# Performance work log

Hardware: AMD Instinct MI355X
Metric: run time of the kernel (lower is better)

The kernel has to match this reference:

```python
import jax, jax.numpy as jnp
import numpy as np

R = 32          # voxel resolution
GROUPS = 8
EPS = 1e-5


def silu(x):
    return x * jax.nn.sigmoid(x)


def group_norm(x, gamma, beta):
    # x: (B, C, *spatial); normalize over (C/G, *spatial) per group
    B, C = x.shape[0], x.shape[1]
    sp = x.shape[2:]
    xg = x.reshape(B, GROUPS, C // GROUPS, -1)
    mean = xg.mean(axis=(2, 3), keepdims=True)
    var = xg.var(axis=(2, 3), keepdims=True)
    xn = ((xg - mean) * jax.lax.rsqrt(var + EPS)).reshape(B, C, *sp)
    pshape = (1, C) + (1,) * len(sp)
    return xn * gamma.reshape(pshape) + beta.reshape(pshape)


def voxelize(x, coords):
    # x: (B, C, N), coords: (B, N, 3) in [0, 1] -> scatter-mean onto (B, C, R, R, R)
    c = coords * (R - 1)
    idx = jnp.clip(jnp.floor(c).astype(jnp.int32), 0, R - 1)
    flat = (idx[..., 0] * R + idx[..., 1]) * R + idx[..., 2]  # (B, N)

    def one(feat_cn, fi):
        sums = jax.ops.segment_sum(feat_cn.T, fi, num_segments=R ** 3)        # (R^3, C)
        cnt = jax.ops.segment_sum(jnp.ones_like(fi, dtype=feat_cn.dtype), fi,
                                  num_segments=R ** 3)                        # (R^3,)
        mean = sums / jnp.clip(cnt, 1.0)[:, None]
        return mean.T.reshape(feat_cn.shape[0], R, R, R)

    return jax.vmap(one)(x, flat)


def devoxelize(vox, coords):
    # vox: (B, C, R, R, R), coords: (B, N, 3) -> trilinear gather (B, C, N)
    B, C = vox.shape[0], vox.shape[1]
    c = coords * (R - 1)
    f = c - jnp.floor(c)                                  # fractional part (B, N, 3)
    x0 = jnp.clip(jnp.floor(c).astype(jnp.int32), 0, R - 1)
    x1 = jnp.clip(x0 + 1, 0, R - 1)
    vflat = vox.reshape(B, C, R ** 3)
    out = jnp.zeros((B, C, coords.shape[1]), dtype=vox.dtype)
    for dx in (0, 1):
        for dy in (0, 1):
            for dz in (0, 1):
                ix = x1[..., 0] if dx else x0[..., 0]
                iy = x1[..., 1] if dy else x0[..., 1]
                iz = x1[..., 2] if dz else x0[..., 2]
                w = ((f[..., 0] if dx else 1.0 - f[..., 0])
                     * (f[..., 1] if dy else 1.0 - f[..., 1])
                     * (f[..., 2] if dz else 1.0 - f[..., 2]))  # (B, N)
                fi = (ix * R + iy) * R + iz                      # (B, N)
                g = jnp.take_along_axis(vflat, fi[:, None, :], axis=2)  # (B, C, N)
                out = out + g * w[:, None, :]
    return out


def conv3d(x, w):
    # x: (B, C, D, H, W), w: (O, I, 3, 3, 3), padding 1
    return jax.lax.conv_general_dilated(
        x, w, window_strides=(1, 1, 1), padding='SAME',
        dimension_numbers=('NCDHW', 'OIDHW', 'NCDHW'))


def setup_inputs() -> dict:
    key = jax.random.key(0)
    ks = jax.random.split(key, 16)
    B, Cin, Cout, N, T = 4, 32, 64, 32768, 256
    s = 0.02
    return {
        'feats_bcn': jax.random.normal(ks[0], (B, Cin, N), jnp.float32),
        'coords_bnc3': jax.random.uniform(ks[1], (B, N, 3), jnp.float32),
        't_emb_bt': jax.random.normal(ks[2], (B, T), jnp.float32),
        'w_in': jax.random.normal(ks[3], (Cout, Cin), jnp.float32) * s,
        'gn1_g': jnp.ones((Cout,), jnp.float32), 'gn1_b': jnp.zeros((Cout,), jnp.float32),
        'w_time': jax.random.normal(ks[4], (Cout, T), jnp.float32) * s,
        'b_time': jnp.zeros((Cout,), jnp.float32),
        'w_vox1': jax.random.normal(ks[5], (Cout, Cout, 3, 3, 3), jnp.float32) * s,
        'gn2_g': jnp.ones((Cout,), jnp.float32), 'gn2_b': jnp.zeros((Cout,), jnp.float32),
        'w_vox2': jax.random.normal(ks[6], (Cout, Cout, 3, 3, 3), jnp.float32) * s,
        'gn3_g': jnp.ones((Cout,), jnp.float32), 'gn3_b': jnp.zeros((Cout,), jnp.float32),
        'w_fuse': jax.random.normal(ks[7], (Cout, Cout), jnp.float32) * s,
        'gn4_g': jnp.ones((Cout,), jnp.float32), 'gn4_b': jnp.zeros((Cout,), jnp.float32),
        'w_skip': jax.random.normal(ks[8], (Cout, Cin), jnp.float32) * s,
    }


def reference(feats_bcn, coords_bnc3, t_emb_bt, w_in, gn1_g, gn1_b, w_time, b_time,
              w_vox1, gn2_g, gn2_b, w_vox2, gn3_g, gn3_b, w_fuse, gn4_g, gn4_b, w_skip):
    # point_in: 1x1 conv1d + GN + SiLU
    x_in = silu(group_norm(jnp.einsum('oc,bcn->bon', w_in, feats_bcn), gn1_g, gn1_b))
    # time bias
    bias = (t_emb_bt @ w_time.T + b_time)[:, :, None]          # (B, C, 1)
    x_in = x_in + bias
    # scatter-mean voxelization + bias
    vox = voxelize(x_in, coords_bnc3) + bias[..., None, None]  # (B, C, R, R, R)
    # voxel conv stack
    vox = silu(group_norm(conv3d(vox, w_vox1), gn2_g, gn2_b))
    vox = silu(group_norm(conv3d(vox, w_vox2), gn3_g, gn3_b))
    # trilinear devoxelize back to points
    devox = devoxelize(vox, coords_bnc3)                        # (B, C, N)
    out = silu(group_norm(jnp.einsum('oc,bcn->bon', w_fuse, devox), gn4_g, gn4_b))
    x_skip = jnp.einsum('oc,bcn->bon', w_skip, feats_bcn)
    return out + x_skip
```

## Files before the change

### kernel.cpp

```cpp
#include <hip/hip_runtime.h>
#include <hip/hip_bf16.h>
#include <hip/hip_fp16.h>

typedef __hip_bfloat16 bf16;
typedef unsigned short u16;
typedef unsigned int u32;
typedef __attribute__((ext_vector_type(8))) short bf16x8;
typedef __attribute__((ext_vector_type(4))) float f32x4;

#define DI __device__ __forceinline__

DI float bfu2f(u32 u) { u32 v = u << 16; float f; __builtin_memcpy(&f, &v, 4); return f; }
DI u16 f2bfu(float f) { bf16 h = __float2bfloat16(f); u16 u; __builtin_memcpy(&u, &h, 2); return u; }
DI float hu2f(u32 u) { __half h; u16 s = (u16)u; __builtin_memcpy(&h, &s, 2); return __half2float(h); }
DI u16 f2hu(float f) { __half h = __float2half(f); u16 u; __builtin_memcpy(&u, &h, 2); return u; }
DI float silu_f(float x) { return x / (1.0f + __expf(-x)); }
DI float ldin(const void* p, long i, int bf) {
  return bf ? bfu2f(((const u16*)p)[i]) : ((const float*)p)[i];
}
DI int detect_bf(const void* g) { return ((*(const u32*)g) & 0xFFFFu) == 0x3F80u; }
DI void unpack8(uint4 q, float* o) {
  o[0] = bfu2f(q.x & 0xFFFFu); o[1] = bfu2f(q.x >> 16);
  o[2] = bfu2f(q.y & 0xFFFFu); o[3] = bfu2f(q.y >> 16);
  o[4] = bfu2f(q.z & 0xFFFFu); o[5] = bfu2f(q.z >> 16);
  o[6] = bfu2f(q.w & 0xFFFFu); o[7] = bfu2f(q.w >> 16);
}
DI void unpack8h(uint4 q, float* o) {
  o[0] = hu2f(q.x & 0xFFFFu); o[1] = hu2f(q.x >> 16);
  o[2] = hu2f(q.y & 0xFFFFu); o[3] = hu2f(q.y >> 16);
  o[4] = hu2f(q.z & 0xFFFFu); o[5] = hu2f(q.z >> 16);
  o[6] = hu2f(q.w & 0xFFFFu); o[7] = hu2f(q.w >> 16);
}
DI uint4 pack8(const float* s) {
  uint4 q;
  q.x = (u32)f2bfu(s[0]) | ((u32)f2bfu(s[1]) << 16);
  q.y = (u32)f2bfu(s[2]) | ((u32)f2bfu(s[3]) << 16);
  q.z = (u32)f2bfu(s[4]) | ((u32)f2bfu(s[5]) << 16);
  q.w = (u32)f2bfu(s[6]) | ((u32)f2bfu(s[7]) << 16);
  return q;
}


__global__ void k_prep(const void* __restrict__ w_in, const void* __restrict__ w_fuse,
                       const void* __restrict__ w_skip, const void* __restrict__ wv1,
                       const void* __restrict__ wv2,
                       const void* __restrict__ g1g, const void* __restrict__ g1b,
                       const void* __restrict__ g2g, const void* __restrict__ g2b,
                       const void* __restrict__ g3g, const void* __restrict__ g3b,
                       const void* __restrict__ g4g, const void* __restrict__ g4b,
                       const void* __restrict__ t_emb, const void* __restrict__ w_time,
                       const void* __restrict__ b_time,
                       float* __restrict__ wT_in, float* __restrict__ wT_fuse,
                       float* __restrict__ wT_skip, u16* __restrict__ wM1,
                       u16* __restrict__ wM2, float* __restrict__ gnp,
                       u16* __restrict__ wFuseM, float* __restrict__ biasb) {
  int bf = detect_bf(g1g);
  int id = blockIdx.x * 256 + threadIdx.x;
  if (id < 2048) { int c = id >> 6, o = id & 63; wT_in[id] = ldin(w_in, o * 32 + c, bf); return; }
  id -= 2048;
  if (id < 4096) { int o = id >> 6, p = id & 63; wT_fuse[id] = ldin(w_fuse, p * 64 + o, bf); return; }
  id -= 4096;
  if (id < 2048) { int c = id >> 6, p = id & 63; wT_skip[id] = ldin(w_skip, p * 32 + c, bf); return; }
  id -= 2048;
  if (id < 110592) {
    int j = id & 7, l = (id >> 3) & 63, f = (id >> 9) & 7, t = id >> 12;
    int o = (f & 3) * 16 + (l & 15);
    int c = (f >> 2) * 32 + ((l >> 4) & 3) * 8 + j;
    wM1[id] = f2bfu(ldin(wv1, (o * 64 + c) * 27 + t, bf));
    return;
  }
  id -= 110592;
  if (id < 110592) {
    int j = id & 7, l = (id >> 3) & 63, f = (id >> 9) & 7, t = id >> 12;
    int o = (f & 3) * 16 + (l & 15);
    int c = (f >> 2) * 32 + ((l >> 4) & 3) * 8 + j;
    wM2[id] = f2bfu(ldin(wv2, (o * 64 + c) * 27 + t, bf));
    return;
  }
  id -= 110592;
  if (id < 512) {
    int stage = id >> 7, j = id & 127;
    const void* src;
    if (stage == 0) src = (j < 64) ? g1g : g1b;
    else if (stage == 1) src = (j < 64) ? g2g : g2b;
    else if (stage == 2) src = (j < 64) ? g3g : g3b;
    else src = (j < 64) ? g4g : g4b;
    gnp[id] = ldin(src, j & 63, bf);
    return;
  }
  id -= 512;
  if (id < 4096) {
    int kh = id >> 11, nt = (id >> 9) & 3, l = (id >> 3) & 63, j = id & 7;
    int o = nt * 16 + (l & 15);
    int k = kh * 32 + ((l >> 4) & 3) * 8 + j;
    wFuseM[id] = f2bfu(ldin(w_fuse, o * 64 + k, bf));
    return;
  }
  id -= 4096;
  if (id < 256) {
    int b = id >> 6, o = id & 63;
    float s = ldin(b_time, o, bf);
    for (int t = 0; t < 256; ++t)
      s += ldin(t_emb, b * 256 + t, bf) * ldin(w_time, o * 256 + t, bf);
    biasb[id] = s;
  }
}

__global__ void k_points(const void* __restrict__ coords, int4* __restrict__ pt4,
                         int* __restrict__ pt_vox, int* __restrict__ counts,
                         const void* __restrict__ g1g) {
  int bf = detect_bf(g1g);
  int id = blockIdx.x * 256 + threadIdx.x;
  int b = id >> 15;
  float cx = ldin(coords, (long)id * 3 + 0, bf) * 31.f;
  float cy = ldin(coords, (long)id * 3 + 1, bf) * 31.f;
  float cz = ldin(coords, (long)id * 3 + 2, bf) * 31.f;
  int x0 = min(max((int)floorf(cx), 0), 31);
  int y0 = min(max((int)floorf(cy), 0), 31);
  int z0 = min(max((int)floorf(cz), 0), 31);
  int x1 = min(x0 + 1, 31), y1 = min(y0 + 1, 31), z1 = min(z0 + 1, 31);
  int pack = x0 | (y0 << 5) | (z0 << 10) | (x1 << 15) | (y1 << 20) | (z1 << 25);
  int4 r;
  r.x = pack;
  float fx = cx - floorf(cx), fy = cy - floorf(cy), fz = cz - floorf(cz);
  __builtin_memcpy(&r.y, &fx, 4);
  __builtin_memcpy(&r.z, &fy, 4);
  __builtin_memcpy(&r.w, &fz, 4);
  pt4[id] = r;
  int fi = (x0 << 10) + (y0 << 5) + z0;
  int bv = (b << 15) + fi;
  pt_vox[id] = bv;
  atomicAdd(counts + bv, 1);
}

__global__ void k_scan1(const int* __restrict__ cnt, int* __restrict__ starts,
                        int* __restrict__ bsum) {
  __shared__ int ls[256];
  int t = threadIdx.x;
  int base = blockIdx.x * 1024 + t * 4;
  int4 c = *(const int4*)(cnt + base);
  int s = c.x + c.y + c.z + c.w;
  ls[t] = s;
  __syncthreads();
  for (int off = 1; off < 256; off <<= 1) {
    int u = (t >= off) ? ls[t - off] : 0;
    __syncthreads();
    ls[t] += u;
    __syncthreads();
  }
  int excl = ls[t] - s;
  starts[base] = excl;
  starts[base + 1] = excl + c.x;
  starts[base + 2] = excl + c.x + c.y;
  starts[base + 3] = excl + c.x + c.y + c.z;
  if (t == 255) bsum[blockIdx.x] = ls[255];
}

__global__ void k_scan3(int* __restrict__ starts, const int* __restrict__ bsum,
                        int* __restrict__ cursor) {
  __shared__ int bp[128];
  int t = threadIdx.x;
  int v0 = (t < 128) ? bsum[t] : 0;
  if (t < 128) bp[t] = v0;
  __syncthreads();
  for (int off = 1; off < 128; off <<= 1) {
    int u = (t >= off && t < 128) ? bp[t - off] : 0;
    __syncthreads();
    if (t < 128) bp[t] += u;
    __syncthreads();
  }
  if (t < 128) bp[t] -= v0;
  __syncthreads();
  int i = blockIdx.x * 256 + t;
  int v = starts[i] + bp[i >> 10];
  starts[i] = v;
  cursor[i] = v;
}

__global__ void k_fill(const int* __restrict__ pt_vox, const int4* __restrict__ pt4,
                       int* __restrict__ cursor, int* __restrict__ list,
                       int4* __restrict__ ptS, int* __restrict__ pid2slot) {
  int id = blockIdx.x * 256 + threadIdx.x;
  int slot = atomicAdd(cursor + pt_vox[id], 1);
  list[slot] = id;
  ptS[slot] = pt4[id];
  pid2slot[id] = slot;
}

__global__ void __launch_bounds__(256, 2) k_xin(const void* __restrict__ feats,
                      const float* __restrict__ wT_in, const int* __restrict__ pid2slot,
                      u16* __restrict__ out, float* __restrict__ gs,
                      const void* __restrict__ g1g) {
  __shared__ float xs[4][16];
  int bf = detect_bf(g1g);
  int tid = threadIdx.x;
  int id = blockIdx.x * 256 + tid;
  int b = id >> 15, n = id & 32767;
  float acc[64];
#pragma unroll
  for (int o = 0; o < 64; ++o) acc[o] = 0.f;
  long base = ((long)b << 20) + n;
  for (int c = 0; c < 32; ++c) {
    float fv = ldin(feats, base + ((long)c << 15), bf);
    const float* wr = wT_in + (c << 6);
#pragma unroll
    for (int o = 0; o < 64; ++o) acc[o] += wr[o] * fv;
  }
  int slot = pid2slot[id];
  uint4* op = (uint4*)(out + ((size_t)slot << 6));
#pragma unroll
  for (int j = 0; j < 8; ++j) op[j] = pack8(acc + j * 8);
  float ps[8], pq[8];
#pragma unroll
  for (int g = 0; g < 8; ++g) {
    float s = 0.f, q = 0.f;
#pragma unroll
    for (int k = 0; k < 8; ++k) { float v = acc[g * 8 + k]; s += v; q += v * v; }
    ps[g] = s; pq[g] = q;
  }
#pragma unroll
  for (int m = 1; m < 64; m <<= 1)
#pragma unroll
    for (int g = 0; g < 8; ++g) {
      ps[g] += __shfl_xor(ps[g], m);
      pq[g] += __shfl_xor(pq[g], m);
    }
  int lane = tid & 63, wv = tid >> 6;
  if (lane == 0) {
#pragma unroll
    for (int g = 0; g < 8; ++g) { xs[wv][g * 2] = ps[g]; xs[wv][g * 2 + 1] = pq[g]; }
  }
  __syncthreads();
  if (tid < 16) {
    float t = xs[0][tid] + xs[1][tid] + xs[2][tid] + xs[3][tid];
    atomicAdd(gs + (blockIdx.x & 7) * 64 + ((b * 8 + (tid >> 1)) << 1) + (tid & 1), t);
  }
}

DI void stats_inline(const float* __restrict__ gsumB, int b, int tid, float* st) {
  if (tid < 8) {
    float s = 0.f, q = 0.f;
    int bg = b * 8 + tid;
#pragma unroll
    for (int bin = 0; bin < 8; ++bin) {
      s += gsumB[bin * 64 + bg * 2];
      q += gsumB[bin * 64 + bg * 2 + 1];
    }
    float mean = s * (1.0f / 262144.0f);
    float var = q * (1.0f / 262144.0f) - mean * mean;
    st[tid * 2] = mean;
    st[tid * 2 + 1] = rsqrtf(fmaxf(var, 0.f) + 1e-5f);
  }
}

__global__ void k_gather(const u16* __restrict__ xmulS, const int* __restrict__ starts,
                         const int* __restrict__ cnt, const float* __restrict__ gsumB,
                         const float* __restrict__ gnp0,
                         const float* __restrict__ bias, u16* __restrict__ voxout) {
  __shared__ float st[16];
  int tid = threadIdx.x;
  int id = blockIdx.x * 256 + tid;
  int j = id & 7;
  int bv = id >> 3;
  int b = bv >> 15;
  stats_inline(gsumB, b, tid, st);
  __syncthreads();
  int s = starts[bv], c = cnt[bv];
  float m = st[j * 2], r = st[j * 2 + 1];
  float acc[8] = {0.f, 0.f, 0.f, 0.f, 0.f, 0.f, 0.f, 0.f};
  for (int k = 0; k < c; ++k) {
    uint4 q = *(const uint4*)(xmulS + ((size_t)(s + k) << 6) + j * 8);
    float x[8];
    unpack8(q, x);
#pragma unroll
    for (int t = 0; t < 8; ++t)
      acc[t] += silu_f((x[t] - m) * r * gnp0[j * 8 + t] + gnp0[64 + j * 8 + t]);
  }
  float inv = 1.0f / fmaxf((float)c, 1.0f);
  float bmul = c ? 2.0f : 1.0f;
  float out[8];
#pragma unroll
  for (int t = 0; t < 8; ++t)
    out[t] = acc[t] * inv + bmul * bias[b * 64 + j * 8 + t];
  *(uint4*)(voxout + ((size_t)bv << 6) + j * 8) = pack8(out);
}

__global__ void __launch_bounds__(256, 2) k_mconv(const u16* __restrict__ in,
                                                  const u16* __restrict__ wM,
                                                  u16* __restrict__ out,
                                                  const u16* __restrict__ zrow,
                                                  float* __restrict__ gs) {
  __shared__ u16 alds[39168];
  int orig = blockIdx.x;
  int wid = (orig & 7) * 128 + (orig >> 3);
  int bin = orig & 7;
  int b = wid >> 8;
  int a0 = (wid >> 3) & 31;
  int a1base = (wid & 7) << 2;
  int tid = threadIdx.x;
  int wave = tid >> 6, lane = tid & 63;
  int quad = lane >> 4, lrow = lane & 15;
  int a1row = a1base + wave;
  const u16* inb = in + ((size_t)b << 21);
  f32x4 acc[2][4] = {};

  for (int it = 0; it < 20; ++it) {
    int cbase = it * 256 + wave * 64;
    int chunk = cbase + lane;
    if (chunk < 4896) {
      int r = chunk >> 3, p = chunk & 7;
      int p0 = r / 204, rem = r - p0 * 204;
      int p1 = rem / 34, n2i = rem - p1 * 34;
      int n0 = a0 + p0 - 1, n1 = a1base + p1 - 1, n2 = n2i - 1;
      bool ok = ((unsigned)n0 < 32u) && ((unsigned)n1 < 32u) && ((unsigned)n2 < 32u);
      int co = (p ^ (r & 7)) << 3;
      const u16* src = ok ? inb + (((size_t)((n0 << 10) + (n1 << 5) + n2)) << 6) + co
                          : zrow + co;
      __builtin_amdgcn_global_load_lds(
          (const __attribute__((address_space(1))) void*)src,
          (__attribute__((address_space(3))) void*)(alds + ((size_t)cbase << 3)), 16, 0, 0);
    }
  }
  asm volatile("s_waitcnt vmcnt(0)" ::: "memory");
  __builtin_amdgcn_s_barrier();

#define LOADW(W, T) { \
  const u16* wp = wM + ((size_t)(T) << 12) + (lane << 3); \
  _Pragma("unroll") for (int f = 0; f < 8; ++f) \
    W[f >> 2][f & 3] = *(const bf16x8*)(wp + (f << 9)); \
}
#define COMPUTE(T2, W) { \
  int rb = (t0 * 6 + wave + t1) * 34 + (T2); \
  _Pragma("unroll") for (int mt = 0; mt < 2; ++mt) { \
    int r = rb + mt * 16 + lrow; \
    int sw = (r & 7) << 3; \
    const u16* rp = alds + r * 64; \
    _Pragma("unroll") for (int kh = 0; kh < 2; ++kh) { \
      bf16x8 a = *(const bf16x8*)(rp + (((kh * 4 + quad) << 3) ^ sw)); \
      _Pragma("unroll") for (int nt = 0; nt < 4; ++nt) \
        acc[mt][nt] = __builtin_amdgcn_mfma_f32_16x16x32_bf16(a, W[kh][nt], acc[mt][nt], 0, 0, 0); \
    } \
  } \
}

  bf16x8 w0[2][4], w1[2][4], w2[2][4];
  LOADW(w0, 0);
  LOADW(w1, 1);
  int t0 = 0, t1 = 0;
#pragma unroll 1
  for (int g = 0; g < 9; ++g) {
    int tb = g * 3;
    LOADW(w2, tb + 2);
    COMPUTE(0, w0);
    if (tb + 3 < 27) LOADW(w0, tb + 3);
    COMPUTE(1, w1);
    if (tb + 4 < 27) LOADW(w1, tb + 4);
    COMPUTE(2, w2);
    ++t1;
    if (t1 == 3) { t1 = 0; ++t0; }
  }
#undef LOADW
#undef COMPUTE

  size_t vbase = ((size_t)b << 15) + (a0 << 10) + (a1row << 5);
#pragma unroll
  for (int mt = 0; mt < 2; ++mt) {
#pragma unroll
    for (int nt = 0; nt < 4; ++nt)
#pragma unroll
      for (int r = 0; r < 4; ++r)
        out[((vbase + mt * 16 + quad * 4 + r) << 6) + nt * 16 + lrow] = f2hu(acc[mt][nt][r]);
  }

  float s[4], q[4];
#pragma unroll
  for (int nt = 0; nt < 4; ++nt) {
    float ss = 0.f, qq = 0.f;
#pragma unroll
    for (int mt = 0; mt < 2; ++mt)
#pragma unroll
      for (int r = 0; r < 4; ++r) { float v = acc[mt][nt][r]; ss += v; qq += v * v; }
    s[nt] = ss; q[nt] = qq;
  }
#pragma unroll
  for (int mi = 0; mi < 5; ++mi) {
    const int masks[5] = {1, 2, 4, 16, 32};
    int m = masks[mi];
#pragma unroll
    for (int nt = 0; nt < 4; ++nt) {
      s[nt] += __shfl_xor(s[nt], m);
      q[nt] += __shfl_xor(q[nt], m);
    }
  }
  __syncthreads();
  float* fs = (float*)&alds[0];
  int par = lrow >> 3;
  if (quad == 0 && (lrow & 7) == 0) {
#pragma unroll
    for (int nt = 0; nt < 4; ++nt) {
      fs[wave * 16 + ((nt * 2 + par) << 1)] = s[nt];
      fs[wave * 16 + ((nt * 2 + par) << 1) + 1] = q[nt];
    }
  }
  __syncthreads();
  if (tid < 16) {
    float t = fs[tid] + fs[16 + tid] + fs[32 + tid] + fs[48 + tid];
    atomicAdd(gs + bin * 64 + ((b * 8 + (tid >> 1)) << 1) + (tid & 1), t);
  }
}

__global__ void k_gnapply(const u16* __restrict__ src, const float* __restrict__ gsumB,
                          const float* __restrict__ gnp, u16* __restrict__ dst) {
  __shared__ float st[16];
  int tid = threadIdx.x;
  int id = blockIdx.x * 256 + tid;
  int j = id & 7;
  int bv = id >> 3;
  int b = bv >> 15;
  stats_inline(gsumB, b, tid, st);
  __syncthreads();
  const u16* ip = src + ((size_t)bv << 6) + j * 8;
  float x[8];
  unpack8h(*(const uint4*)ip, x);
  float m = st[j * 2], r = st[j * 2 + 1];
#pragma unroll
  for (int k = 0; k < 8; ++k)
    x[k] = silu_f((x[k] - m) * r * gnp[j * 8 + k] + gnp[64 + j * 8 + k]);
  *(uint4*)(dst + ((size_t)bv << 6) + j * 8) = pack8(x);
}

__global__ void __launch_bounds__(256, 4) k_devoxfuse(const u16* __restrict__ vox,
                       const int4* __restrict__ ptS, const int* __restrict__ list,
                       const u16* __restrict__ wFuseM,
                       u16* __restrict__ dst, float* __restrict__ gs) {
  __shared__ int lsl[256];
  __shared__ float fsh[4][16];
  int tid = threadIdx.x;
  int wave = tid >> 6, lane = tid & 63;
  int quad = lane >> 4, lrow = lane & 15;
  int blk = blockIdx.x;
  int b = blk >> 7;
  int bin = blk & 7;
  lsl[tid] = list[blk * 256 + tid];
  bf16x8 bF[2][4];
#pragma unroll
  for (int kh = 0; kh < 2; ++kh)
#pragma unroll
    for (int nt = 0; nt < 4; ++nt)
      bF[kh][nt] = *(const bf16x8*)(wFuseM + ((kh * 4 + nt) * 64 + lane) * 8);
  __syncthreads();
  const u16* vb = vox + ((size_t)b << 21) + quad * 8;
  float sr[4] = {0.f, 0.f, 0.f, 0.f}, qr[4] = {0.f, 0.f, 0.f, 0.f};

#pragma unroll 1
  for (int i = 0; i < 4; ++i) {
    int sbase = blk * 256 + wave * 64 + i * 16;
    int4 pt = ptS[sbase + lrow];
    int pk = pt.x;
    int x0 = pk & 31, y0 = (pk >> 5) & 31, z0 = (pk >> 10) & 31;
    int x1 = (pk >> 15) & 31, y1 = (pk >> 20) & 31, z1 = (pk >> 25) & 31;
    float fx, fy, fz;
    __builtin_memcpy(&fx, &pt.y, 4);
    __builtin_memcpy(&fy, &pt.z, 4);
    __builtin_memcpy(&fz, &pt.w, 4);
    float facc[16];
#pragma unroll
    for (int t = 0; t < 16; ++t) facc[t] = 0.f;
#pragma unroll
    for (int dx = 0; dx < 2; ++dx) {
      int ixc = dx ? x1 : x0;
      float wx = dx ? fx : 1.f - fx;
#pragma unroll
      for (int dy = 0; dy < 2; ++dy) {
        int iyc = dy ? y1 : y0;
        float wxy = wx * (dy ? fy : 1.f - fy);
#pragma unroll
        for (int dz = 0; dz < 2; ++dz) {
          int izc = dz ? z1 : z0;
          float w = wxy * (dz ? fz : 1.f - fz);
          const u16* p = vb + ((size_t)((ixc << 10) + (iyc << 5) + izc) << 6);
          float v0[8], v1[8];
          unpack8(*(const uint4*)p, v0);
          unpack8(*(const uint4*)(p + 32), v1);
#pragma unroll
          for (int t = 0; t < 8; ++t) { facc[t] += w * v0[t]; facc[8 + t] += w * v1[t]; }
        }
      }
    }
    bf16x8 a0, a1;
#pragma unroll
    for (int t = 0; t < 8; ++t) {
      a0[t] = (short)f2bfu(facc[t]);
      a1[t] = (short)f2bfu(facc[8 + t]);
    }
    f32x4 acc4[4] = {};
#pragma unroll
    for (int nt = 0; nt < 4; ++nt)
      acc4[nt] = __builtin_amdgcn_mfma_f32_16x16x32_bf16(a0, bF[0][nt], acc4[nt], 0, 0, 0);
#pragma unroll
    for (int nt = 0; nt < 4; ++nt)
      acc4[nt] = __builtin_amdgcn_mfma_f32_16x16x32_bf16(a1, bF[1][nt], acc4[nt], 0, 0, 0);
    int4 pids = *(const int4*)&lsl[wave * 64 + i * 16 + quad * 4];
    int pid_[4] = {pids.x, pids.y, pids.z, pids.w};
#pragma unroll
    for (int nt = 0; nt < 4; ++nt) {
#pragma unroll
      for (int r = 0; r < 4; ++r) {
        float v = acc4[nt][r];
        dst[((size_t)pid_[r] << 6) + nt * 16 + lrow] = f2bfu(v);
        sr[nt] += v; qr[nt] += v * v;
      }
    }
  }

#pragma unroll
  for (int mi = 0; mi < 5; ++mi) {
    const int masks[5] = {1, 2, 4, 16, 32};
    int m = masks[mi];
#pragma unroll
    for (int nt = 0; nt < 4; ++nt) {
      sr[nt] += __shfl_xor(sr[nt], m);
      qr[nt] += __shfl_xor(qr[nt], m);
    }
  }
  int par = lrow >> 3;
  if (quad == 0 && (lrow & 7) == 0) {
#pragma unroll
    for (int nt = 0; nt < 4; ++nt) {
      fsh[wave][(nt * 2 + par) << 1] = sr[nt];
      fsh[wave][((nt * 2 + par) << 1) + 1] = qr[nt];
    }
  }
  __syncthreads();
  if (tid < 16) {
    float t = fsh[0][tid] + fsh[1][tid] + fsh[2][tid] + fsh[3][tid];
    atomicAdd(gs + bin * 64 + ((b * 8 + (tid >> 1)) << 1) + (tid & 1), t);
  }
}

__global__ void __launch_bounds__(256, 2) k_final(const u16* __restrict__ y,
                        const float* __restrict__ gsumB,
                        const float* __restrict__ gnp3, const void* __restrict__ feats,
                        const float* __restrict__ wT_skip, float* __restrict__ out,
                        const void* __restrict__ g1g) {
  __shared__ float st[16];
  int bf = detect_bf(g1g);
  int tid = threadIdx.x;
  int id = blockIdx.x * 256 + tid;
  int b = id >> 15, n = id & 32767;
  stats_inline(gsumB, b, tid, st);
  __syncthreads();
  const uint4* yr = (const uint4*)(y + ((size_t)id << 6));
  float r[64];
#pragma unroll
  for (int j = 0; j < 8; ++j) unpack8(yr[j], r + j * 8);
#pragma unroll
  for (int o = 0; o < 64; ++o) {
    int g = o >> 3;
    r[o] = silu_f((r[o] - st[g * 2]) * st[g * 2 + 1] * gnp3[o] + gnp3[64 + o]);
  }
  long base = ((long)b << 20) + n;
  for (int c = 0; c < 32; ++c) {
    float fv = ldin(feats, base + ((long)c << 15), bf);
    const float* wr = wT_skip + (c << 6);
#pragma unroll
    for (int p = 0; p < 64; ++p) r[p] += wr[p] * fv;
  }
  float* op = out + ((size_t)b << 21) + n;
#pragma unroll
  for (int p = 0; p < 64; ++p) op[(size_t)p << 15] = r[p];
}

extern "C" void kernel_launch(void* const* d_in, const int* in_sizes, int n_in,
                              void* d_out, int out_size, void* d_ws, size_t ws_size,
                              hipStream_t stream) {
  const void* feats  = d_in[0];
  const void* coords = d_in[1];
  const void* t_emb  = d_in[2];
  const void* w_in   = d_in[3];
  const void* gn1_g  = d_in[4];
  const void* gn1_b  = d_in[5];
  const void* w_time = d_in[6];
  const void* b_time = d_in[7];
  const void* w_vox1 = d_in[8];
  const void* gn2_g  = d_in[9];
  const void* gn2_b  = d_in[10];
  const void* w_vox2 = d_in[11];
  const void* gn3_g  = d_in[12];
  const void* gn3_b  = d_in[13];
  const void* w_fuse = d_in[14];
  const void* gn4_g  = d_in[15];
  const void* gn4_b  = d_in[16];
  const void* w_skip = d_in[17];

  u16* S = (u16*)d_out;

  char* ws = (char*)d_ws;
  u16*   BufP    = (u16*)  (ws + 0);
  u16*   VoxB    = (u16*)  (ws + 16777216);
  int*   counts  = (int*)  (ws + 33554432);
  float* gsumB   = (float*)(ws + 34078720);
  u16*   zpad    = (u16*)  (ws + 34086912);
  int4*  pt4     = (int4*) (ws + 34087168);
  int*   pt_vox  = (int*)  (ws + 36184320);
  int*   starts  = (int*)  (ws + 36708608);
  int*   cursor  = (int*)  (ws + 37232896);
  int*   list    = (int*)  (ws + 37757184);
  int4*  ptS     = (int4*) (ws + 38281472);
  int*   bsum    = (int*)  (ws + 40378624);
  float* biasb   = (float*)(ws + 40379136);
  float* gnp     = (float*)(ws + 40380160);
  float* wT_in   = (float*)(ws + 40382208);
  float* wT_fuse = (float*)(ws + 40390400);
  float* wT_skip = (float*)(ws + 40406784);
  u16*   wM1     = (u16*)  (ws + 40414976);
  u16*   wM2     = (u16*)  (ws + 40636160);
  u16*   wFuseM  = (u16*)  (ws + 40857344);
  int*   pid2slot= (int*)  (ws + 40865536);

  hipMemsetAsync(counts, 0, 532736, stream);

  k_prep<<<915, 256, 0, stream>>>(w_in, w_fuse, w_skip, w_vox1, w_vox2,
                                  gn1_g, gn1_b, gn2_g, gn2_b, gn3_g, gn3_b,
                                  gn4_g, gn4_b, t_emb, w_time, b_time,
                                  wT_in, wT_fuse, wT_skip, wM1, wM2, gnp,
                                  wFuseM, biasb);
  k_points<<<512, 256, 0, stream>>>(coords, pt4, pt_vox, counts, gn1_g);
  k_scan1<<<128, 256, 0, stream>>>(counts, starts, bsum);
  k_scan3<<<512, 256, 0, stream>>>(starts, bsum, cursor);
  k_fill<<<512, 256, 0, stream>>>(pt_vox, pt4, cursor, list, ptS, pid2slot);
  k_xin<<<512, 256, 0, stream>>>(feats, wT_in, pid2slot, BufP, gsumB + 0, gn1_g);
  k_gather<<<4096, 256, 0, stream>>>(BufP, starts, counts, gsumB + 0,
                                     gnp + 0, biasb, VoxB);
  k_mconv<<<1024, 256, 0, stream>>>(VoxB, wM1, S, zpad, gsumB + 512);
  k_gnapply<<<4096, 256, 0, stream>>>(S, gsumB + 512, gnp + 128, BufP);
  k_mconv<<<1024, 256, 0, stream>>>(BufP, wM2, S, zpad, gsumB + 1024);
  k_gnapply<<<4096, 256, 0, stream>>>(S, gsumB + 1024, gnp + 256, VoxB);
  k_devoxfuse<<<512, 256, 0, stream>>>(VoxB, ptS, list, wFuseM, BufP, gsumB + 1536);
  k_final<<<512, 256, 0, stream>>>(BufP, gsumB + 1536, gnp + 384, feats, wT_skip,
                                   (float*)d_out, gn1_g);
}
```

Before: 342.0 us.

## Split conv3d taps across waves with LDS cross-wave reduction instead of rows

The 3x3x3 conv kernel now has each wave handle a subset of the 27 taps for all 4 output rows, rather than all 27 taps for one row. Each weight tile is loaded once per block instead of by every wave, cutting weight-load traffic fourfold. The price is a 4x larger accumulator array (128 floats per lane), which raises register pressure and may spill or lower occupancy under launch_bounds(256,2). It also adds a two-phase cross-wave reduction through LDS with extra barriers, and waves get uneven work (7 vs 6 taps).

After: 1.193 ms. 249% more time.

```diff
diff --git a/kernel.cpp b/kernel.cpp
--- a/kernel.cpp
+++ b/kernel.cpp
@@ -290,7 +290,7 @@
                                                   u16* __restrict__ out,
                                                   const u16* __restrict__ zrow,
                                                   float* __restrict__ gs) {
-  __shared__ u16 alds[39168];
+  __shared__ __align__(16) u16 alds[39168];
   int orig = blockIdx.x;
   int wid = (orig & 7) * 128 + (orig >> 3);
   int bin = orig & 7;
@@ -300,9 +300,8 @@
   int tid = threadIdx.x;
   int wave = tid >> 6, lane = tid & 63;
   int quad = lane >> 4, lrow = lane & 15;
-  int a1row = a1base + wave;
   const u16* inb = in + ((size_t)b << 21);
-  f32x4 acc[2][4] = {};
+  f32x4 acc[8][4] = {};
 
   for (int it = 0; it < 20; ++it) {
     int cbase = it * 256 + wave * 64;
@@ -329,47 +328,73 @@
   _Pragma("unroll") for (int f = 0; f < 8; ++f) \
     W[f >> 2][f & 3] = *(const bf16x8*)(wp + (f << 9)); \
 }
-#define COMPUTE(T2, W) { \
-  int rb = (t0 * 6 + wave + t1) * 34 + (T2); \
-  _Pragma("unroll") for (int mt = 0; mt < 2; ++mt) { \
-    int r = rb + mt * 16 + lrow; \
+#define COMPUTE_TAP(T, W) { \
+  int t0_ = (T) / 9, r9_ = (T) - t0_ * 9; \
+  int t1_ = r9_ / 3, t2_ = r9_ - t1_ * 3; \
+  _Pragma("unroll") for (int m = 0; m < 8; ++m) { \
+    int r = (t0_ * 6 + (m >> 1) + t1_) * 34 + t2_ + ((m & 1) << 4) + lrow; \
     int sw = (r & 7) << 3; \
     const u16* rp = alds + r * 64; \
     _Pragma("unroll") for (int kh = 0; kh < 2; ++kh) { \
-      bf16x8 a = *(const bf16x8*)(rp + (((kh * 4 + quad) << 3) ^ sw)); \
+      bf16x8 a = *(const bf16x8*)(rp + ((((kh << 2) + quad) << 3) ^ sw)); \
       _Pragma("unroll") for (int nt = 0; nt < 4; ++nt) \
-        acc[mt][nt] = __builtin_amdgcn_mfma_f32_16x16x32_bf16(a, W[kh][nt], acc[mt][nt], 0, 0, 0); \
+        acc[m][nt] = __builtin_amdgcn_mfma_f32_16x16x32_bf16(a, W[kh][nt], acc[m][nt], 0, 0, 0); \
     } \
   } \
 }
 
-  bf16x8 w0[2][4], w1[2][4], w2[2][4];
-  LOADW(w0, 0);
-  LOADW(w1, 1);
-  int t0 = 0, t1 = 0;
+  int nT = (wave < 3) ? 7 : 6;
+  bf16x8 wA[2][4], wB[2][4];
+  LOADW(wA, wave);
 #pragma unroll 1
-  for (int g = 0; g < 9; ++g) {
-    int tb = g * 3;
-    LOADW(w2, tb + 2);
-    COMPUTE(0, w0);
-    if (tb + 3 < 27) LOADW(w0, tb + 3);
-    COMPUTE(1, w1);
-    if (tb + 4 < 27) LOADW(w1, tb + 4);
-    COMPUTE(2, w2);
-    ++t1;
-    if (t1 == 3) { t1 = 0; ++t0; }
+  for (int k = 0; k < nT; ++k) {
+    int t = wave + (k << 2);
+    if ((k & 1) == 0) {
+      if (k + 1 < nT) LOADW(wB, t + 4);
+      COMPUTE_TAP(t, wA);
+    } else {
+      if (k + 1 < nT) LOADW(wA, t + 4);
+      COMPUTE_TAP(t, wB);
+    }
   }
 #undef LOADW
-#undef COMPUTE
-
-  size_t vbase = ((size_t)b << 15) + (a0 << 10) + (a1row << 5);
-#pragma unroll
-  for (int mt = 0; mt < 2; ++mt) {
+#undef COMPUTE_TAP
+
+  float* red = (float*)&alds[0];
+#pragma unroll 1
+  for (int ph = 0; ph < 2; ++ph) {
+    __syncthreads();
+    int mb = ph << 2;
+#pragma unroll
+    for (int mi = 0; mi < 4; ++mi)
+#pragma unroll
+      for (int nt = 0; nt < 4; ++nt)
+        *(f32x4*)(red + (((wave << 4) + (mi << 2) + nt) << 8) + (lane << 2)) = acc[mb + mi][nt];
+    __syncthreads();
+    if ((wave >> 1) == ph) {
+      int mi0 = (wave & 1) << 1;
+#pragma unroll
+      for (int mi = mi0; mi < mi0 + 2; ++mi)
+#pragma unroll
+        for (int nt = 0; nt < 4; ++nt) {
+          f32x4 s0 = *(const f32x4*)(red + (((0 << 4) + (mi << 2) + nt) << 8) + (lane << 2));
+          f32x4 s1 = *(const f32x4*)(red + (((1 << 4) + (mi << 2) + nt) << 8) + (lane << 2));
+          f32x4 s2 = *(const f32x4*)(red + (((2 << 4) + (mi << 2) + nt) << 8) + (lane << 2));
+          f32x4 s3 = *(const f32x4*)(red + (((3 << 4) + (mi << 2) + nt) << 8) + (lane << 2));
+          acc[mb + mi][nt] = (s0 + s1) + (s2 + s3);
+        }
+    }
+  }
+
+  size_t vbase = ((size_t)b << 15) + (a0 << 10) + ((size_t)(a1base + wave) << 5);
+#pragma unroll
+  for (int mi = 0; mi < 2; ++mi) {
+    int m = (wave << 1) + mi;
 #pragma unroll
     for (int nt = 0; nt < 4; ++nt)
 #pragma unroll
       for (int r = 0; r < 4; ++r)
-        out[((vbase + mt * 16 + quad * 4 + r) << 6) + nt * 16 + lrow] = f2hu(acc[mt][nt][r]);
+        out[((vbase + mi * 16 + quad * 4 + r) << 6) + nt * 16 + lrow] = f2hu(acc[m][nt][r]);
   }
 
   float s[4], q[4];
@@ -377,9 +402,11 @@
   for (int nt = 0; nt < 4; ++nt) {
     float ss = 0.f, qq = 0.f;
 #pragma unroll
-    for (int mt = 0; mt < 2; ++mt)
-#pragma unroll
-      for (int r = 0; r < 4; ++r) { float v = acc[mt][nt][r]; ss += v; qq += v * v; }
+    for (int mi = 0; mi < 2; ++mi) {
+      int m = (wave << 1) + mi;
+#pragma unroll
+      for (int r = 0; r < 4; ++r) { float v = acc[m][nt][r]; ss += v; qq += v * v; }
+    }
     s[nt] = ss; q[nt] = qq;
   }
 #pragma unroll
```
